# Kernel optimization log

Measured on AMD Instinct MI355X. Metric: run time of the kernel, lower is better.

The kernel has to match this reference:

```python
import jax, jax.numpy as jnp
import numpy as np

N = 8192
E = 512
EPS = 1e-12  # F.normalize default eps


def setup_inputs() -> dict:
    key = jax.random.key(0)
    ks = jax.random.split(key, 7)
    scale = 1.0 / np.sqrt(E)  # roughly match nn.Linear init scale
    return {
        "x": jax.random.normal(ks[0], (N, E), dtype=jnp.float32),
        "Wq": jax.random.normal(ks[1], (E, E), dtype=jnp.float32) * scale,
        "bq": jax.random.normal(ks[2], (E,), dtype=jnp.float32) * scale,
        "Wk": jax.random.normal(ks[3], (E, E), dtype=jnp.float32) * scale,
        "bk": jax.random.normal(ks[4], (E,), dtype=jnp.float32) * scale,
        "Wv": jax.random.normal(ks[5], (E, E), dtype=jnp.float32) * scale,
        "bv": jax.random.normal(ks[6], (E,), dtype=jnp.float32) * scale,
    }


def reference(x, Wq, bq, Wk, bk, Wv, bv):
    # torch nn.Linear: y = x @ W^T + b
    q = x @ Wq.T + bq  # [N, E]
    k = x @ Wk.T + bk  # [N, E]
    v = x @ Wv.T + bv  # [N, E]
    s = q @ k.T  # [N, N]
    # F.normalize(s): L2-normalize each row (dim=1), norm clamped to eps
    norm = jnp.maximum(jnp.linalg.norm(s, axis=1, keepdims=True), EPS)
    w = s / norm
    # F.softmax default dim for 2-D input is dim=1
    w = jax.nn.softmax(w, axis=1)
    return w @ v  # [N, E]
```

## Files before the change

kernel.cpp:

```cpp
#include <hip/hip_runtime.h>
#include <hip/hip_bf16.h>

typedef unsigned short u16;
typedef unsigned int u32;
typedef short short8 __attribute__((ext_vector_type(8)));
typedef float fvec4 __attribute__((ext_vector_type(4)));

#define NR 8192
#define ED 512
#define PSTR 264

__device__ inline u16 f2bf(float f) {
    union { float f; unsigned u; } c; c.f = f;
    unsigned u = c.u;
    u += 0x7FFFu + ((u >> 16) & 1u);
    return (u16)(u >> 16);
}
__device__ inline float bf2f(u16 h) {
    union { unsigned u; float f; } c; c.u = ((unsigned)h) << 16; return c.f;
}
__device__ inline short8 load_cvt8(const float* p) {
    const fvec4* q = (const fvec4*)p;
    fvec4 a = q[0], b = q[1];
    short8 r;
    r[0] = (short)f2bf(a[0]); r[1] = (short)f2bf(a[1]);
    r[2] = (short)f2bf(a[2]); r[3] = (short)f2bf(a[3]);
    r[4] = (short)f2bf(b[0]); r[5] = (short)f2bf(b[1]);
    r[6] = (short)f2bf(b[2]); r[7] = (short)f2bf(b[3]);
    return r;
}
__device__ inline void gload16(const void* g, void* l) {
    __builtin_amdgcn_global_load_lds(
        (const __attribute__((address_space(1))) u32*)g,
        (__attribute__((address_space(3))) u32*)l, 16, 0, 0);
}

#define SWZ_SCOL(lane) ((((lane) & 7) ^ ((lane) >> 3)) * 8)
#define SWZ_RD(col, row) ((col) ^ (((row) & 7) * 8))

__global__ __launch_bounds__(256) void cvt_kernel(
    const float* __restrict__ x, const float* __restrict__ Wq,
    const float* __restrict__ Wk, const float* __restrict__ Wv,
    u16* __restrict__ xb, u16* __restrict__ wb)
{
    int tid = blockIdx.x * 256 + threadIdx.x;
    const float* src; u16* dst; int off;
    if (tid < 524288)      { src = x;  dst = xb;          off = tid; }
    else if (tid < 557056) { src = Wq; dst = wb;          off = tid - 524288; }
    else if (tid < 589824) { src = Wk; dst = wb + 262144; off = tid - 557056; }
    else                   { src = Wv; dst = wb + 524288; off = tid - 589824; }
    *(short8*)(dst + (size_t)off * 8) = load_cvt8(src + (size_t)off * 8);
}

__global__ __launch_bounds__(256, 3) void qkv_kernel(
    const u16* __restrict__ xb, const u16* __restrict__ wb,
    const float* __restrict__ bq, const float* __restrict__ bk, const float* __restrict__ bv,
    u16* __restrict__ qb, u16* __restrict__ kb, u16* __restrict__ kT, u16* __restrict__ vT)
{
    __shared__ u16 ldsA[128][64];
    __shared__ u16 ldsB[128][64];

    const int lane = threadIdx.x & 63;
    const int w = threadIdx.x >> 6;
    const int ln = lane & 15;
    const int kg = lane >> 4;
    const int wr = w >> 1, wc = w & 1;
    const int z = blockIdx.z;
    const int R0 = blockIdx.y * 128;
    const int C0 = blockIdx.x * 128;
    const int srow = lane >> 3;
    const int scol = SWZ_SCOL(lane);

    const u16* B = wb + (size_t)z * 262144;
    const float* bias = (z == 0) ? bq : (z == 1) ? bk : bv;

    fvec4 acc[4][4];
    #pragma unroll
    for (int m = 0; m < 4; ++m)
        #pragma unroll
        for (int n = 0; n < 4; ++n) acc[m][n] = (fvec4){0.f, 0.f, 0.f, 0.f};

    for (int kt = 0; kt < 8; ++kt) {
        const int k0 = kt * 64;
        __syncthreads();
        #pragma unroll
        for (int i = 0; i < 4; ++i) {
            const int ra = (i * 4 + w) * 8;
            gload16(xb + (size_t)(R0 + ra + srow) * ED + k0 + scol, &ldsA[ra][0]);
            gload16(B  + (size_t)(C0 + ra + srow) * ED + k0 + scol, &ldsB[ra][0]);
        }
        __syncthreads();
        short8 af[2][4], bf8[2][4];
        #pragma unroll
        for (int kk = 0; kk < 2; ++kk) {
            #pragma unroll
            for (int m = 0; m < 4; ++m) {
                const int row = wr * 64 + m * 16 + ln;
                af[kk][m] = *(const short8*)&ldsA[row][SWZ_RD(kk * 32 + kg * 8, row)];
            }
            #pragma unroll
            for (int n = 0; n < 4; ++n) {
                const int row = wc * 64 + n * 16 + ln;
                bf8[kk][n] = *(const short8*)&ldsB[row][SWZ_RD(kk * 32 + kg * 8, row)];
            }
        }
        #pragma unroll
        for (int kk = 0; kk < 2; ++kk)
            #pragma unroll
            for (int m = 0; m < 4; ++m)
                #pragma unroll
                for (int n = 0; n < 4; ++n)
                    acc[m][n] = __builtin_amdgcn_mfma_f32_16x16x32_bf16(af[kk][m], bf8[kk][n], acc[m][n], 0, 0, 0);
    }

    #pragma unroll
    for (int n = 0; n < 4; ++n) {
        const int gcol = C0 + wc * 64 + n * 16 + ln;
        const float bc = bias[gcol];
        #pragma unroll
        for (int m = 0; m < 4; ++m) {
            #pragma unroll
            for (int r = 0; r < 4; ++r) {
                const int grow = R0 + wr * 64 + m * 16 + kg * 4 + r;
                u16 val = f2bf(acc[m][n][r] + bc);
                if (z == 0) {
                    qb[(size_t)grow * ED + gcol] = val;
                } else if (z == 1) {
                    kb[(size_t)grow * ED + gcol] = val;
                    kT[(size_t)gcol * NR + grow] = val;
                } else {
                    vT[(size_t)gcol * NR + grow] = val;
                }
            }
        }
    }
}

__global__ __launch_bounds__(256) void gram_kernel(
    const u16* __restrict__ kT, u16* __restrict__ Gb)
{
    __shared__ float red[4][64][4];
    const int lane = threadIdx.x & 63;
    const int w = threadIdx.x >> 6;
    const int ln = lane & 15;
    const int kg = lane >> 4;
    const int i0 = (blockIdx.x >> 5) * 16, l0 = (blockIdx.x & 31) * 16;

    fvec4 acc[4];
    #pragma unroll
    for (int c = 0; c < 4; ++c) acc[c] = (fvec4){0.f, 0.f, 0.f, 0.f};
    const u16* arow = kT + (size_t)(i0 + ln) * NR + w * 2048 + kg * 8;
    const u16* brow = kT + (size_t)(l0 + ln) * NR + w * 2048 + kg * 8;
    #pragma unroll 8
    for (int t = 0; t < 64; ++t) {
        acc[t & 3] = __builtin_amdgcn_mfma_f32_16x16x32_bf16(
            *(const short8*)(arow + t * 32), *(const short8*)(brow + t * 32), acc[t & 3], 0, 0, 0);
    }
    fvec4 s = acc[0] + acc[1] + acc[2] + acc[3];
    #pragma unroll
    for (int r = 0; r < 4; ++r) red[w][lane][r] = s[r];
    __syncthreads();
    if (w == 0) {
        #pragma unroll
        for (int r = 0; r < 4; ++r) {
            float tot = red[0][lane][r] + red[1][lane][r] + red[2][lane][r] + red[3][lane][r];
            Gb[(size_t)(i0 + kg * 4 + r) * ED + l0 + ln] = f2bf(tot);
        }
    }
}

__global__ __launch_bounds__(256) void rn_kernel(
    const u16* __restrict__ qb, const u16* __restrict__ Gb, float* __restrict__ rn)
{
    __shared__ float red[4][16];
    const int lane = threadIdx.x & 63;
    const int wv = threadIdx.x >> 6;
    const int ln = lane & 15;
    const int kg = lane >> 4;
    const int m0 = blockIdx.x * 16;

    short8 afr[16];
    const u16* qrow = qb + (size_t)(m0 + ln) * ED + kg * 8;
    #pragma unroll
    for (int t = 0; t < 16; ++t) afr[t] = *(const short8*)(qrow + t * 32);

    float ss[4] = {0.f, 0.f, 0.f, 0.f};
    for (int ee = 0; ee < 8; ++ee) {
        const int e = wv * 8 + ee;
        fvec4 a0 = (fvec4){0.f, 0.f, 0.f, 0.f};
        fvec4 a1 = (fvec4){0.f, 0.f, 0.f, 0.f};
        const u16* grow = Gb + (size_t)(e * 16 + ln) * ED + kg * 8;
        #pragma unroll
        for (int t = 0; t < 16; t += 2) {
            a0 = __builtin_amdgcn_mfma_f32_16x16x32_bf16(afr[t],     *(const short8*)(grow + t * 32),       a0, 0, 0, 0);
            a1 = __builtin_amdgcn_mfma_f32_16x16x32_bf16(afr[t + 1], *(const short8*)(grow + (t + 1) * 32), a1, 0, 0, 0);
        }
        fvec4 acc = a0 + a1;
        #pragma unroll
        for (int r = 0; r < 4; ++r)
            ss[r] += acc[r] * bf2f(qb[(size_t)(m0 + kg * 4 + r) * ED + e * 16 + ln]);
    }
    #pragma unroll
    for (int r = 0; r < 4; ++r) {
        float v = ss[r];
        v += __shfl_xor(v, 1); v += __shfl_xor(v, 2);
        v += __shfl_xor(v, 4); v += __shfl_xor(v, 8);
        ss[r] = v;
    }
    if (ln == 0) {
        #pragma unroll
        for (int r = 0; r < 4; ++r) red[wv][kg * 4 + r] = ss[r];
    }
    __syncthreads();
    if (threadIdx.x < 16) {
        const int row = threadIdx.x;
        const float tot = red[0][row] + red[1][row] + red[2][row] + red[3][row];
        rn[m0 + row] = 1.0f / fmaxf(sqrtf(tot), 1e-12f);
    }
}

__global__ __launch_bounds__(256, 3) void sexp_kernel(
    const u16* __restrict__ qb, const u16* __restrict__ kb,
    const float* __restrict__ rn, u16* __restrict__ P, float* __restrict__ dsum)
{
    __shared__ u16 ldsA[128][64];
    __shared__ u16 ldsB[128][64];

    const int lane = threadIdx.x & 63;
    const int w = threadIdx.x >> 6;
    const int ln = lane & 15;
    const int kg = lane >> 4;
    const int wr = w >> 1, wc = w & 1;
    const int R0 = blockIdx.y * 128;
    const int C0 = blockIdx.x * 128;
    const int srow = lane >> 3;
    const int scol = SWZ_SCOL(lane);

    fvec4 acc[4][4];
    #pragma unroll
    for (int m = 0; m < 4; ++m)
        #pragma unroll
        for (int n = 0; n < 4; ++n) acc[m][n] = (fvec4){0.f, 0.f, 0.f, 0.f};

    for (int kt = 0; kt < 8; ++kt) {
        const int k0 = kt * 64;
        __syncthreads();
        #pragma unroll
        for (int i = 0; i < 4; ++i) {
            const int ra = (i * 4 + w) * 8;
            gload16(qb + (size_t)(R0 + ra + srow) * ED + k0 + scol, &ldsA[ra][0]);
            gload16(kb + (size_t)(C0 + ra + srow) * ED + k0 + scol, &ldsB[ra][0]);
        }
        __syncthreads();
        short8 af[2][4], bf8[2][4];
        #pragma unroll
        for (int kk = 0; kk < 2; ++kk) {
            #pragma unroll
            for (int m = 0; m < 4; ++m) {
                const int row = wr * 64 + m * 16 + ln;
                af[kk][m] = *(const short8*)&ldsA[row][SWZ_RD(kk * 32 + kg * 8, row)];
            }
            #pragma unroll
            for (int n = 0; n < 4; ++n) {
                const int row = wc * 64 + n * 16 + ln;
                bf8[kk][n] = *(const short8*)&ldsB[row][SWZ_RD(kk * 32 + kg * 8, row)];
            }
        }
        #pragma unroll
        for (int kk = 0; kk < 2; ++kk)
            #pragma unroll
            for (int m = 0; m < 4; ++m)
                #pragma unroll
                for (int n = 0; n < 4; ++n)
                    acc[m][n] = __builtin_amdgcn_mfma_f32_16x16x32_bf16(af[kk][m], bf8[kk][n], acc[m][n], 0, 0, 0);
    }

    #pragma unroll
    for (int m = 0; m < 4; ++m) {
        float dpart[4] = {0.f, 0.f, 0.f, 0.f};
        #pragma unroll
        for (int r = 0; r < 4; ++r) {
            const int grow = R0 + wr * 64 + m * 16 + kg * 4 + r;
            const float rv = rn[grow];
            #pragma unroll
            for (int n = 0; n < 4; ++n) {
                const int gcol = C0 + wc * 64 + n * 16 + ln;
                u16 pb = f2bf(__expf(acc[m][n][r] * rv));
                P[(size_t)grow * NR + gcol] = pb;
                dpart[r] += bf2f(pb);
            }
        }
        #pragma unroll
        for (int r = 0; r < 4; ++r) {
            float v = dpart[r];
            v += __shfl_xor(v, 1); v += __shfl_xor(v, 2);
            v += __shfl_xor(v, 4); v += __shfl_xor(v, 8);
            if (ln == 0)
                atomicAdd(&dsum[R0 + wr * 64 + m * 16 + kg * 4 + r], v);
        }
    }
}

__global__ __launch_bounds__(512, 4) void pv256_kernel(
    const u16* __restrict__ P, const u16* __restrict__ vT, float* __restrict__ part,
    int ksteps)
{
    __shared__ u16 ldsA[128][64];
    __shared__ u16 ldsB[256][64];

    const int lane = threadIdx.x & 63;
    const int w = threadIdx.x >> 6;
    const int ln = lane & 15;
    const int kg = lane >> 4;
    const int wr = w >> 2, wc = w & 3;
    const int id2 = blockIdx.y * gridDim.x + blockIdx.x;
    const int tile = ((id2 & 7) << 4) + (id2 >> 3);
    const int R0 = (tile >> 1) * 128;
    const int C0 = (tile & 1) * 256;
    const int ks = blockIdx.z;
    const int srow = lane >> 3;
    const int scol = SWZ_SCOL(lane);

    float* pp = part + (size_t)ks * NR * ED;

    fvec4 acc[4][4];
    #pragma unroll
    for (int m = 0; m < 4; ++m)
        #pragma unroll
        for (int n = 0; n < 4; ++n) acc[m][n] = (fvec4){0.f, 0.f, 0.f, 0.f};

    for (int kt = 0; kt < ksteps; ++kt) {
        const int k0 = (ks * ksteps + kt) * 64;
        __syncthreads();
        #pragma unroll
        for (int i = 0; i < 2; ++i) {
            const int ra = (i * 8 + w) * 8;
            gload16(P + (size_t)(R0 + ra + srow) * NR + k0 + scol, &ldsA[ra][0]);
        }
        #pragma unroll
        for (int i = 0; i < 4; ++i) {
            const int rb = (i * 8 + w) * 8;
            gload16(vT + (size_t)(C0 + rb + srow) * NR + k0 + scol, &ldsB[rb][0]);
        }
        __syncthreads();
        short8 af[2][4], bf8[2][4];
        #pragma unroll
        for (int kk = 0; kk < 2; ++kk) {
            #pragma unroll
            for (int m = 0; m < 4; ++m) {
                const int row = wr * 64 + m * 16 + ln;
                af[kk][m] = *(const short8*)&ldsA[row][SWZ_RD(kk * 32 + kg * 8, row)];
            }
            #pragma unroll
            for (int n = 0; n < 4; ++n) {
                const int row = wc * 64 + n * 16 + ln;
                bf8[kk][n] = *(const short8*)&ldsB[row][SWZ_RD(kk * 32 + kg * 8, row)];
            }
        }
        #pragma unroll
        for (int kk = 0; kk < 2; ++kk)
            #pragma unroll
            for (int m = 0; m < 4; ++m)
                #pragma unroll
                for (int n = 0; n < 4; ++n)
                    acc[m][n] = __builtin_amdgcn_mfma_f32_16x16x32_bf16(af[kk][m], bf8[kk][n], acc[m][n], 0, 0, 0);
    }

    #pragma unroll
    for (int m = 0; m < 4; ++m) {
        #pragma unroll
        for (int r = 0; r < 4; ++r) {
            const int grow = R0 + wr * 64 + m * 16 + kg * 4 + r;
            #pragma unroll
            for (int n = 0; n < 4; ++n) {
                const int gcol = C0 + wc * 64 + n * 16 + ln;
                pp[(size_t)grow * ED + gcol] = acc[m][n][r];
            }
        }
    }
}

__global__ __launch_bounds__(256, 4) void pv_kernel(
    const u16* __restrict__ P, const u16* __restrict__ vT, float* __restrict__ part,
    int ksteps)
{
    __shared__ u16 ldsA[128][64];
    __shared__ u16 ldsB[128][64];

    const int lane = threadIdx.x & 63;
    const int w = threadIdx.x >> 6;
    const int ln = lane & 15;
    const int kg = lane >> 4;
    const int wr = w >> 1, wc = w & 1;
    const int id2 = blockIdx.y * gridDim.x + blockIdx.x;
    const int tile = ((id2 & 7) << 5) + (id2 >> 3);
    const int R0 = (tile >> 2) * 128;
    const int C0 = (tile & 3) * 128;
    const int ks = blockIdx.z;
    const int srow = lane >> 3;
    const int scol = SWZ_SCOL(lane);

    float* pp = part + (size_t)ks * NR * ED;

    fvec4 acc[4][4];
    #pragma unroll
    for (int m = 0; m < 4; ++m)
        #pragma unroll
        for (int n = 0; n < 4; ++n) acc[m][n] = (fvec4){0.f, 0.f, 0.f, 0.f};

    for (int kt = 0; kt < ksteps; ++kt) {
        const int k0 = (ks * ksteps + kt) * 64;
        __syncthreads();
        #pragma unroll
        for (int i = 0; i < 4; ++i) {
            const int ra = (i * 4 + w) * 8;
            gload16(P  + (size_t)(R0 + ra + srow) * NR + k0 + scol, &ldsA[ra][0]);
            gload16(vT + (size_t)(C0 + ra + srow) * NR + k0 + scol, &ldsB[ra][0]);
        }
        __syncthreads();
        short8 af[2][4], bf8[2][4];
        #pragma unroll
        for (int kk = 0; kk < 2; ++kk) {
            #pragma unroll
            for (int m = 0; m < 4; ++m) {
                const int row = wr * 64 + m * 16 + ln;
                af[kk][m] = *(const short8*)&ldsA[row][SWZ_RD(kk * 32 + kg * 8, row)];
            }
            #pragma unroll
            for (int n = 0; n < 4; ++n) {
                const int row = wc * 64 + n * 16 + ln;
                bf8[kk][n] = *(const short8*)&ldsB[row][SWZ_RD(kk * 32 + kg * 8, row)];
            }
        }
        #pragma unroll
        for (int kk = 0; kk < 2; ++kk)
            #pragma unroll
            for (int m = 0; m < 4; ++m)
                #pragma unroll
                for (int n = 0; n < 4; ++n)
                    acc[m][n] = __builtin_amdgcn_mfma_f32_16x16x32_bf16(af[kk][m], bf8[kk][n], acc[m][n], 0, 0, 0);
    }

    #pragma unroll
    for (int m = 0; m < 4; ++m) {
        #pragma unroll
        for (int r = 0; r < 4; ++r) {
            const int grow = R0 + wr * 64 + m * 16 + kg * 4 + r;
            #pragma unroll
            for (int n = 0; n < 4; ++n) {
                const int gcol = C0 + wc * 64 + n * 16 + ln;
                pp[(size_t)grow * ED + gcol] = acc[m][n][r];
            }
        }
    }
}

__global__ __launch_bounds__(256) void reduce_kernel(
    const float* __restrict__ part, const float* __restrict__ dsum,
    float* __restrict__ out, int nsplit)
{
    const size_t idx = ((size_t)blockIdx.x * 256 + threadIdx.x) * 4;
    const int row = (int)(idx >> 9);
    const float iv = 1.0f / dsum[row];
    fvec4 s = *(const fvec4*)(part + idx);
    for (int k = 1; k < nsplit; ++k) {
        fvec4 b = *(const fvec4*)(part + (size_t)k * NR * ED + idx);
        #pragma unroll
        for (int i = 0; i < 4; ++i) s[i] += b[i];
    }
    fvec4 o;
    #pragma unroll
    for (int i = 0; i < 4; ++i) o[i] = s[i] * iv;
    *(fvec4*)(out + idx) = o;
}

__global__ __launch_bounds__(512, 2) void attn_kernel(
    const u16* __restrict__ qb, const u16* __restrict__ kb,
    const u16* __restrict__ vT, const float* __restrict__ rn, float* __restrict__ out)
{
    __shared__ u16 p_lds[2 * 16 * PSTR];
    __shared__ float red[2][4][16];

    const int lane = threadIdx.x & 63;
    const int w = threadIdx.x >> 6;
    const int ln = lane & 15;
    const int kg = lane >> 4;
    const int rh = w >> 2;
    const int jg = w & 3;
    const int R0 = blockIdx.x * 32 + rh * 16;

    short8 afr[16];
    const u16* qrow = qb + (size_t)(R0 + ln) * ED + kg * 8;
    #pragma unroll
    for (int t = 0; t < 16; ++t) afr[t] = *(const short8*)(qrow + t * 32);

    float rnv[4];
    #pragma unroll
    for (int r = 0; r < 4; ++r) rnv[r] = rn[R0 + kg * 4 + r];

    fvec4 oacc[8];
    #pragma unroll
    for (int e = 0; e < 8; ++e) oacc[e] = (fvec4){0.f, 0.f, 0.f, 0.f};
    float dsum[4] = {0.f, 0.f, 0.f, 0.f};

    u16* pw = p_lds + rh * 16 * PSTR;

    for (int c = 0; c < 32; ++c) {
        const int j0 = c * 256 + jg * 64;
        fvec4 acc[4];
        #pragma unroll
        for (int jt = 0; jt < 4; ++jt) acc[jt] = (fvec4){0.f, 0.f, 0.f, 0.f};
        const u16* kbase = kb + (size_t)(j0 + ln) * ED + kg * 8;
        #pragma unroll 4
        for (int t = 0; t < 16; ++t) {
            short8 af = afr[t];
            #pragma unroll
            for (int jt = 0; jt < 4; ++jt) {
                short8 bfr = *(const short8*)(kbase + (size_t)jt * 16 * ED + t * 32);
                acc[jt] = __builtin_amdgcn_mfma_f32_16x16x32_bf16(af, bfr, acc[jt], 0, 0, 0);
            }
        }
        #pragma unroll
        for (int jt = 0; jt < 4; ++jt) {
            #pragma unroll
            for (int r = 0; r < 4; ++r) {
                float p = __expf(acc[jt][r] * rnv[r]);
                dsum[r] += p;
                pw[(kg * 4 + r) * PSTR + jg * 64 + jt * 16 + ln] = f2bf(p);
            }
        }
        __syncthreads();
        const u16* vbase = vT + (size_t)(jg * 128 + ln) * NR + c * 256 + kg * 8;
        const u16* prow = pw + ln * PSTR + kg * 8;
        #pragma unroll
        for (int kk = 0; kk < 8; ++kk) {
            short8 afp = *(const short8*)(prow + kk * 32);
            #pragma unroll
            for (int e = 0; e < 8; ++e) {
                short8 bfr = *(const short8*)(vbase + (size_t)e * 16 * NR + kk * 32);
                oacc[e] = __builtin_amdgcn_mfma_f32_16x16x32_bf16(afp, bfr, oacc[e], 0, 0, 0);
            }
        }
        __syncthreads();
    }

    #pragma unroll
    for (int r = 0; r < 4; ++r) {
        float v = dsum[r];
        v += __shfl_xor(v, 1); v += __shfl_xor(v, 2);
        v += __shfl_xor(v, 4); v += __shfl_xor(v, 8);
        dsum[r] = v;
    }
    if (ln == 0) {
        #pragma unroll
        for (int r = 0; r < 4; ++r) red[rh][jg][kg * 4 + r] = dsum[r];
    }
    __syncthreads();
    float inv[4];
    #pragma unroll
    for (int r = 0; r < 4; ++r) {
        const int row = kg * 4 + r;
        inv[r] = 1.0f / (red[rh][0][row] + red[rh][1][row] + red[rh][2][row] + red[rh][3][row]);
    }
    #pragma unroll
    for (int e = 0; e < 8; ++e) {
        #pragma unroll
        for (int r = 0; r < 4; ++r)
            out[(size_t)(R0 + kg * 4 + r) * ED + jg * 128 + e * 16 + ln] = oacc[e][r] * inv[r];
    }
}

extern "C" void kernel_launch(void* const* d_in, const int* in_sizes, int n_in,
                              void* d_out, int out_size, void* d_ws, size_t ws_size,
                              hipStream_t stream) {
    const float* x  = (const float*)d_in[0];
    const float* Wq = (const float*)d_in[1];
    const float* bq = (const float*)d_in[2];
    const float* Wk = (const float*)d_in[3];
    const float* bk = (const float*)d_in[4];
    const float* Wv = (const float*)d_in[5];
    const float* bv = (const float*)d_in[6];
    float* out = (float*)d_out;

    u16* xb = (u16*)d_ws;
    u16* wb = xb + (size_t)NR * ED;
    u16* qb = wb + 3 * 262144;
    u16* kb = qb + (size_t)NR * ED;
    u16* kT = kb + (size_t)NR * ED;
    u16* vT = kT + (size_t)NR * ED;
    u16* Gb = vT + (size_t)NR * ED;
    float* rn   = (float*)(Gb + 262144);
    float* dsum = rn + NR;
    u16* P = (u16*)(dsum + NR);

    const size_t need = (size_t)((u16*)(dsum + NR) - (u16*)d_ws) * 2 + (size_t)NR * NR * 2;
    const size_t need4 = need + (size_t)4 * NR * ED * sizeof(float);

    cvt_kernel<<<2432, 256, 0, stream>>>(x, Wq, Wk, Wv, xb, wb);
    dim3 g1(ED / 128, NR / 128, 3);
    qkv_kernel<<<g1, 256, 0, stream>>>(xb, wb, bq, bk, bv, qb, kb, kT, vT);
    gram_kernel<<<1024, 256, 0, stream>>>(kT, Gb);
    rn_kernel<<<512, 256, 0, stream>>>(qb, Gb, rn);

    if (ws_size >= need) {
        hipMemsetAsync(dsum, 0, NR * sizeof(float), stream);
        dim3 gs(NR / 128, NR / 128);
        sexp_kernel<<<gs, 256, 0, stream>>>(qb, kb, rn, P, dsum);

        if (ws_size >= need4) {
            float* part = (float*)(P + (size_t)NR * NR);
            dim3 gp(ED / 256, NR / 128, 4);
            pv256_kernel<<<gp, 512, 0, stream>>>(P, vT, part, 32);
            reduce_kernel<<<NR * ED / 4 / 256, 256, 0, stream>>>(part, dsum, out, 4);
        } else {
            float* part = (float*)d_ws;
            dim3 gp(ED / 128, NR / 128, 2);
            pv_kernel<<<gp, 256, 0, stream>>>(P, vT, part, 64);
            reduce_kernel<<<NR * ED / 4 / 256, 256, 0, stream>>>(part, dsum, out, 2);
        }
    } else {
        attn_kernel<<<NR / 32, 512, 0, stream>>>(qb, kb, vT, rn, out);
    }
}
```

Before: 328.9 us.

## Stage K/V transposes through LDS and store split-K partials in bf16

The QKV epilogue for K and V now writes tiles into a padded LDS buffer, shared with the staging buffers through a union. Each thread then writes contiguous 16-byte rows into kT/vT, replacing scattered 2-byte transposed global stores. The split-K PV partials are now stored as bf16 instead of fp32, halving partial traffic, and the reduce kernel handles 8 elements per thread. The cost is extra rounding error on the partial sums, and the LDS transpose adds syncs to the QKV epilogue.

```diff
diff --git a/kernel.cpp b/kernel.cpp
--- a/kernel.cpp
+++ b/kernel.cpp
@@ -3,12 +3,14 @@
 
 typedef unsigned short u16;
 typedef unsigned int u32;
+typedef short s4v __attribute__((ext_vector_type(4)));
 typedef short short8 __attribute__((ext_vector_type(8)));
 typedef float fvec4 __attribute__((ext_vector_type(4)));
 
 #define NR 8192
 #define ED 512
 #define PSTR 264
+#define TRP 136
 
 __device__ inline u16 f2bf(float f) {
     union { float f; unsigned u; } c; c.f = f;
@@ -57,8 +59,10 @@
     const float* __restrict__ bq, const float* __restrict__ bk, const float* __restrict__ bv,
     u16* __restrict__ qb, u16* __restrict__ kb, u16* __restrict__ kT, u16* __restrict__ vT)
 {
-    __shared__ u16 ldsA[128][64];
-    __shared__ u16 ldsB[128][64];
+    __shared__ union {
+        u16 stage[2][128][64];
+        u16 tr[128 * TRP];
+    } lds;
 
     const int lane = threadIdx.x & 63;
     const int w = threadIdx.x >> 6;
@@ -86,8 +90,8 @@
         #pragma unroll
         for (int i = 0; i < 4; ++i) {
             const int ra = (i * 4 + w) * 8;
-            gload16(xb + (size_t)(R0 + ra + srow) * ED + k0 + scol, &ldsA[ra][0]);
-            gload16(B  + (size_t)(C0 + ra + srow) * ED + k0 + scol, &ldsB[ra][0]);
+            gload16(xb + (size_t)(R0 + ra + srow) * ED + k0 + scol, &lds.stage[0][ra][0]);
+            gload16(B  + (size_t)(C0 + ra + srow) * ED + k0 + scol, &lds.stage[1][ra][0]);
         }
         __syncthreads();
         short8 af[2][4], bf8[2][4];
@@ -96,12 +100,12 @@
             #pragma unroll
             for (int m = 0; m < 4; ++m) {
                 const int row = wr * 64 + m * 16 + ln;
-                af[kk][m] = *(const short8*)&ldsA[row][SWZ_RD(kk * 32 + kg * 8, row)];
+                af[kk][m] = *(const short8*)&lds.stage[0][row][SWZ_RD(kk * 32 + kg * 8, row)];
             }
             #pragma unroll
             for (int n = 0; n < 4; ++n) {
                 const int row = wc * 64 + n * 16 + ln;
-                bf8[kk][n] = *(const short8*)&ldsB[row][SWZ_RD(kk * 32 + kg * 8, row)];
+                bf8[kk][n] = *(const short8*)&lds.stage[1][row][SWZ_RD(kk * 32 + kg * 8, row)];
             }
         }
         #pragma unroll
@@ -113,25 +117,49 @@
                     acc[m][n] = __builtin_amdgcn_mfma_f32_16x16x32_bf16(af[kk][m], bf8[kk][n], acc[m][n], 0, 0, 0);
     }
 
-    #pragma unroll
-    for (int n = 0; n < 4; ++n) {
-        const int gcol = C0 + wc * 64 + n * 16 + ln;
-        const float bc = bias[gcol];
-        #pragma unroll
-        for (int m = 0; m < 4; ++m) {
-            #pragma unroll
-            for (int r = 0; r < 4; ++r) {
-                const int grow = R0 + wr * 64 + m * 16 + kg * 4 + r;
-                u16 val = f2bf(acc[m][n][r] + bc);
-                if (z == 0) {
-                    qb[(size_t)grow * ED + gcol] = val;
-                } else if (z == 1) {
-                    kb[(size_t)grow * ED + gcol] = val;
-                    kT[(size_t)gcol * NR + grow] = val;
-                } else {
-                    vT[(size_t)gcol * NR + grow] = val;
+    if (z == 0) {
+        #pragma unroll
+        for (int n = 0; n < 4; ++n) {
+            const int gcol = C0 + wc * 64 + n * 16 + ln;
+            const float bc = bias[gcol];
+            #pragma unroll
+            for (int m = 0; m < 4; ++m) {
+                #pragma unroll
+                for (int r = 0; r < 4; ++r) {
+                    qb[(size_t)(R0 + wr * 64 + m * 16 + kg * 4 + r) * ED + gcol] = f2bf(acc[m][n][r] + bc);
                 }
             }
+        }
+    } else {
+        __syncthreads();
+        u16* dst = (z == 1) ? kT : vT;
+        #pragma unroll
+        for (int n = 0; n < 4; ++n) {
+            const int col = wc * 64 + n * 16 + ln;
+            const float bc = bias[C0 + col];
+            #pragma unroll
+            for (int m = 0; m < 4; ++m) {
+                const int row0 = wr * 64 + m * 16 + kg * 4;
+                s4v pk;
+                #pragma unroll
+                for (int r = 0; r < 4; ++r) pk[r] = (short)f2bf(acc[m][n][r] + bc);
+                *(s4v*)&lds.tr[col * TRP + row0] = pk;
+                if (z == 1) {
+                    #pragma unroll
+                    for (int r = 0; r < 4; ++r) {
+                        kb[(size_t)(R0 + row0 + r) * ED + C0 + col] = (u16)(unsigned short)pk[r];
+                    }
+                }
+            }
+        }
+        __syncthreads();
+        const int col = threadIdx.x & 127;
+        const int half = threadIdx.x >> 7;
+        u16* drow = dst + (size_t)(C0 + col) * NR + R0 + half * 64;
+        const u16* srow2 = &lds.tr[col * TRP + half * 64];
+        #pragma unroll
+        for (int j = 0; j < 8; ++j) {
+            *(short8*)&drow[j * 8] = *(const short8*)&srow2[j * 8];
         }
     }
 }
@@ -302,7 +330,7 @@
 }
 
 __global__ __launch_bounds__(512, 4) void pv256_kernel(
-    const u16* __restrict__ P, const u16* __restrict__ vT, float* __restrict__ part,
+    const u16* __restrict__ P, const u16* __restrict__ vT, u16* __restrict__ part,
     int ksteps)
 {
     __shared__ u16 ldsA[128][64];
@@ -321,7 +349,7 @@
     const int srow = lane >> 3;
     const int scol = SWZ_SCOL(lane);
 
-    float* pp = part + (size_t)ks * NR * ED;
+    u16* pp = part + (size_t)ks * NR * ED;
 
     fvec4 acc[4][4];
     #pragma unroll
@@ -374,14 +402,14 @@
             #pragma unroll
             for (int n = 0; n < 4; ++n) {
                 const int gcol = C0 + wc * 64 + n * 16 + ln;
-                pp[(size_t)grow * ED + gcol] = acc[m][n][r];
+                pp[(size_t)grow * ED + gcol] = f2bf(acc[m][n][r]);
             }
         }
     }
 }
 
 __global__ __launch_bounds__(256, 4) void pv_kernel(
-    const u16* __restrict__ P, const u16* __restrict__ vT, float* __restrict__ part,
+    const u16* __restrict__ P, const u16* __restrict__ vT, u16* __restrict__ part,
     int ksteps)
 {
     __shared__ u16 ldsA[128][64];
@@ -400,7 +428,7 @@
     const int srow = lane >> 3;
     const int scol = SWZ_SCOL(lane);
 
-    float* pp = part + (size_t)ks * NR * ED;
+    u16* pp = part + (size_t)ks * NR * ED;
 
     fvec4 acc[4][4];
     #pragma unroll
@@ -449,29 +477,30 @@
             #pragma unroll
             for (int n = 0; n < 4; ++n) {
                 const int gcol = C0 + wc * 64 + n * 16 + ln;
-                pp[(size_t)grow * ED + gcol] = acc[m][n][r];
+                pp[(size_t)grow * ED + gcol] = f2bf(acc[m][n][r]);
             }
         }
     }
 }
 
 __global__ __launch_bounds__(256) void reduce_kernel(
-    const float* __restrict__ part, const float* __restrict__ dsum,
+    const u16* __restrict__ part, const float* __restrict__ dsum,
     float* __restrict__ out, int nsplit)
 {
-    const size_t idx = ((size_t)blockIdx.x * 256 + threadIdx.x) * 4;
+    const size_t idx = ((size_t)blockIdx.x * 256 + threadIdx.x) * 8;
     const int row = (int)(idx >> 9);
     const float iv = 1.0f / dsum[row];
-    fvec4 s = *(const fvec4*)(part + idx);
-    for (int k = 1; k < nsplit; ++k) {
-        fvec4 b = *(const fvec4*)(part + (size_t)k * NR * ED + idx);
-        #pragma unroll
-        for (int i = 0; i < 4; ++i) s[i] += b[i];
-    }
-    fvec4 o;
-    #pragma unroll
-    for (int i = 0; i < 4; ++i) o[i] = s[i] * iv;
-    *(fvec4*)(out + idx) = o;
+    float s[8] = {0.f, 0.f, 0.f, 0.f, 0.f, 0.f, 0.f, 0.f};
+    for (int k = 0; k < nsplit; ++k) {
+        short8 v = *(const short8*)(part + (size_t)k * NR * ED + idx);
+        #pragma unroll
+        for (int i = 0; i < 8; ++i) s[i] += bf2f((u16)(unsigned short)v[i]);
+    }
+    fvec4 o0, o1;
+    #pragma unroll
+    for (int i = 0; i < 4; ++i) { o0[i] = s[i] * iv; o1[i] = s[i + 4] * iv; }
+    *(fvec4*)(out + idx) = o0;
+    *(fvec4*)(out + idx + 4) = o1;
 }
 
 __global__ __launch_bounds__(512, 2) void attn_kernel(
@@ -594,7 +623,7 @@
     u16* P = (u16*)(dsum + NR);
 
     const size_t need = (size_t)((u16*)(dsum + NR) - (u16*)d_ws) * 2 + (size_t)NR * NR * 2;
-    const size_t need4 = need + (size_t)4 * NR * ED * sizeof(float);
+    const size_t need4 = need + (size_t)4 * NR * ED * sizeof(u16);
 
     cvt_kernel<<<2432, 256, 0, stream>>>(x, Wq, Wk, Wv, xb, wb);
     dim3 g1(ED / 128, NR / 128, 3);
@@ -608,15 +637,15 @@
         sexp_kernel<<<gs, 256, 0, stream>>>(qb, kb, rn, P, dsum);
 
         if (ws_size >= need4) {
-            float* part = (float*)(P + (size_t)NR * NR);
+            u16* part = P + (size_t)NR * NR;
             dim3 gp(ED / 256, NR / 128, 4);
             pv256_kernel<<<gp, 512, 0, stream>>>(P, vT, part, 32);
-            reduce_kernel<<<NR * ED / 4 / 256, 256, 0, stream>>>(part, dsum, out, 4);
+            reduce_kernel<<<NR * ED / 8 / 256, 256, 0, stream>>>(part, dsum, out, 4);
         } else {
-            float* part = (float*)d_ws;
+            u16* part = (u16*)d_ws;
             dim3 gp(ED / 128, NR / 128, 2);
             pv_kernel<<<gp, 256, 0, stream>>>(P, vT, part, 64);
-            reduce_kernel<<<NR * ED / 4 / 256, 256, 0, stream>>>(part, dsum, out, 2);
+            reduce_kernel<<<NR * ED / 8 / 256, 256, 0, stream>>>(part, dsum, out, 2);
         }
     } else {
         attn_kernel<<<NR / 32, 512, 0, stream>>>(qb, kb, vT, rn, out);
```

After: 314.3 us. 1.05x faster.
